# Optimization experiments

Hardware: AMD Instinct MI355X
Metric: run time of the kernel (lower is better)

## Reference

```python
import jax, jax.numpy as jnp
import numpy as np

# Multi-scale feature pyramid spatial shapes (h, w) per level; static for jit.
SPATIAL_SHAPES = np.array([[64, 176], [32, 88], [16, 44], [8, 22]], dtype=np.int32)


def setup_inputs() -> dict:
    key = jax.random.key(0)
    k1, k2 = jax.random.split(key)
    bs, num_heads, head_dim = 6, 8, 32          # 6 cams, embed_dim 256
    num_queries, num_levels, num_points = 40000, 4, 4  # 200x200 BEV grid, 4 Z anchors
    num_keys = int((SPATIAL_SHAPES[:, 0] * SPATIAL_SHAPES[:, 1]).sum())  # 14960
    value = jax.random.normal(k1, (bs, num_keys, num_heads, head_dim), jnp.float32)
    # normalized sampling locations in [0,1] (x, y)
    sampling_locations = jax.random.uniform(
        k2, (bs, num_queries, num_heads, num_levels, num_points, 2), jnp.float32)
    value_spatial_shapes = jnp.asarray(SPATIAL_SHAPES)
    return {"value": value,
            "value_spatial_shapes": value_spatial_shapes,
            "sampling_locations": sampling_locations}


def _msda(value, sampling_locations):
    """Multi-scale deformable attention, nearest sampling, zero padding,
    align_corners=False (matches F.grid_sample defaults used in the source).
    value: (bs, num_keys, H, D); sampling_locations: (bs, nq, H, L, P, 2).
    Returns (bs, nq, H*D)."""
    bs, _, H, D = value.shape
    _, nq, _, num_levels, P, _ = sampling_locations.shape
    grids = 2.0 * sampling_locations - 1.0  # -> [-1, 1]
    out = jnp.zeros((bs, H, nq, D), value.dtype)
    offset = 0
    for lvl in range(num_levels):
        h, w = int(SPATIAL_SHAPES[lvl, 0]), int(SPATIAL_SHAPES[lvl, 1])
        # (bs, h*w, H, D) -> (bs, H, h*w, D)
        v = jnp.transpose(value[:, offset:offset + h * w], (0, 2, 1, 3))
        g = grids[:, :, :, lvl]                      # (bs, nq, H, P, 2)
        # unnormalize (align_corners=False): pix = ((g+1)*size - 1)/2
        x = (g[..., 0] + 1.0) * w * 0.5 - 0.5
        y = (g[..., 1] + 1.0) * h * 0.5 - 0.5
        ix = jnp.rint(x).astype(jnp.int32)
        iy = jnp.rint(y).astype(jnp.int32)
        valid = (ix >= 0) & (ix < w) & (iy >= 0) & (iy < h)
        idx = jnp.clip(iy, 0, h - 1) * w + jnp.clip(ix, 0, w - 1)  # (bs, nq, H, P)
        idx = jnp.transpose(idx, (0, 2, 1, 3)).reshape(bs, H, nq * P)
        sampled = jnp.take_along_axis(v, idx[..., None], axis=2)  # (bs, H, nq*P, D)
        mask = jnp.transpose(valid, (0, 2, 1, 3)).reshape(bs, H, nq * P, 1)
        sampled = jnp.where(mask, sampled, 0.0).reshape(bs, H, nq, P, D)
        out = out + sampled.sum(axis=3)  # sum over points; accumulating over levels
        offset += h * w
    # (bs, H, nq, D) -> (bs, nq, H*D)
    return jnp.transpose(out, (0, 2, 1, 3)).reshape(bs, nq, H * D)


def reference(value, value_spatial_shapes, sampling_locations):
    # value_spatial_shapes matches the static SPATIAL_SHAPES constant used for
    # level splitting (shapes must be static under jit).
    return _msda(value, sampling_locations)
```

## Files before the change

### kernel.cpp

```cpp
#include <hip/hip_runtime.h>


#define BS 6
#define NQ 40000
#define NH 8
#define HD 32
#define NK 14960

__global__ __launch_bounds__(256)
void msda_kernel(const float* __restrict__ value,
                 const float* __restrict__ loc,
                 float* __restrict__ out) {
    constexpr int Wl[4]  = {176, 88, 44, 22};
    constexpr int Hl[4]  = {64, 32, 16, 8};
    constexpr int Off[4] = {0, 11264, 14080, 14784};

    const int tid = blockIdx.x * 256 + threadIdx.x;
    const int dg  = tid & 7;
    const int g   = tid >> 3;
    const int h   = g & 7;
    const int bq  = g >> 3;
    const int b   = bq / NQ;

    const float4* lp = (const float4*)(loc + (size_t)g * 32);
    const float* vbase = value + (size_t)b * (NK * NH * HD) + h * HD + dg * 4;

    float4 acc = make_float4(0.f, 0.f, 0.f, 0.f);

    #pragma unroll
    for (int l = 0; l < 4; ++l) {
        const int   W  = Wl[l], Hh = Hl[l], off = Off[l];
        const float wf = (float)W, hf = (float)Hh;
        #pragma unroll
        for (int i = 0; i < 2; ++i) {
            const float4 xy2 = lp[l * 2 + i];
            #pragma unroll
            for (int j = 0; j < 2; ++j) {
                const float px = j ? xy2.z : xy2.x;
                const float py = j ? xy2.w : xy2.y;
                const float gx = 2.0f * px - 1.0f;
                const float gy = 2.0f * py - 1.0f;
                const float x  = ((gx + 1.0f) * wf) * 0.5f - 0.5f;
                const float y  = ((gy + 1.0f) * hf) * 0.5f - 0.5f;
                const float fx = rintf(x);
                const float fy = rintf(y);
                const int ix = (int)fx;
                const int iy = (int)fy;
                const bool valid = (ix >= 0) & (ix < W) & (iy >= 0) & (iy < Hh);
                const int cx = min(max(ix, 0), W - 1);
                const int cy = min(max(iy, 0), Hh - 1);
                const int key = off + cy * W + cx;
                const float4 v = *(const float4*)(vbase + (size_t)key * (NH * HD));
                if (valid) {
                    acc.x += v.x; acc.y += v.y; acc.z += v.z; acc.w += v.w;
                }
            }
        }
    }

    *(float4*)(out + (size_t)g * HD + dg * 4) = acc;
}

extern "C" void kernel_launch(void* const* d_in, const int* in_sizes, int n_in,
                              void* d_out, int out_size, void* d_ws, size_t ws_size,
                              hipStream_t stream) {
    const float* value = (const float*)d_in[0];
    const float* loc   = (const float*)d_in[2];
    float* out = (float*)d_out;

    msda_kernel<<<60000, 256, 0, stream>>>(value, loc, out);
}
```

Before: 705.3 us.

## Split index math across lanes, broadcast offsets via shuffle, batch all gathers

Each of the 8 lanes sharing a (query, head) now computes sample indices for only one level/point pair instead of all 16, and the packed byte offsets plus valid bits are exchanged with wavefront shuffles. All 16 value gathers are then issued together, with an empty asm barrier that keeps them in flight at once. Masking becomes an FMA with a 0/1 weight. The aim is to remove redundant index computation and raise memory-level parallelism, at the cost of more registers (occupancy hint 4) and 32-bit unsigned addressing that assumes the value buffer fits in 4 GB.

```diff
diff --git a/kernel.cpp b/kernel.cpp
--- a/kernel.cpp
+++ b/kernel.cpp
@@ -7,14 +7,12 @@
 #define HD 32
 #define NK 14960
 
-__global__ __launch_bounds__(256)
+typedef float f32x4 __attribute__((ext_vector_type(4)));
+
+__global__ __launch_bounds__(256, 4)
 void msda_kernel(const float* __restrict__ value,
                  const float* __restrict__ loc,
                  float* __restrict__ out) {
-    constexpr int Wl[4]  = {176, 88, 44, 22};
-    constexpr int Hl[4]  = {64, 32, 16, 8};
-    constexpr int Off[4] = {0, 11264, 14080, 14784};
-
     const int tid = blockIdx.x * 256 + threadIdx.x;
     const int dg  = tid & 7;
     const int g   = tid >> 3;
@@ -22,43 +20,70 @@
     const int bq  = g >> 3;
     const int b   = bq / NQ;
 
-    const float4* lp = (const float4*)(loc + (size_t)g * 32);
-    const float* vbase = value + (size_t)b * (NK * NH * HD) + h * HD + dg * 4;
+    const int lane = threadIdx.x & 63;
+    const int ll   = lane & 7;
 
-    float4 acc = make_float4(0.f, 0.f, 0.f, 0.f);
+    const f32x4 myL = *(const f32x4*)(loc + (size_t)g * 32 + ll * 4);
 
+    const int l   = ll >> 1;
+    const int W   = 176 >> l;
+    const int Hh  = 64  >> l;
+    const int off = (45056 - (45056 >> (2 * l))) / 3;
+    const float wf = (float)W, hf = (float)Hh;
+
+    int koff[2];
     #pragma unroll
-    for (int l = 0; l < 4; ++l) {
-        const int   W  = Wl[l], Hh = Hl[l], off = Off[l];
-        const float wf = (float)W, hf = (float)Hh;
-        #pragma unroll
-        for (int i = 0; i < 2; ++i) {
-            const float4 xy2 = lp[l * 2 + i];
-            #pragma unroll
-            for (int j = 0; j < 2; ++j) {
-                const float px = j ? xy2.z : xy2.x;
-                const float py = j ? xy2.w : xy2.y;
-                const float gx = 2.0f * px - 1.0f;
-                const float gy = 2.0f * py - 1.0f;
-                const float x  = ((gx + 1.0f) * wf) * 0.5f - 0.5f;
-                const float y  = ((gy + 1.0f) * hf) * 0.5f - 0.5f;
-                const float fx = rintf(x);
-                const float fy = rintf(y);
-                const int ix = (int)fx;
-                const int iy = (int)fy;
-                const bool valid = (ix >= 0) & (ix < W) & (iy >= 0) & (iy < Hh);
-                const int cx = min(max(ix, 0), W - 1);
-                const int cy = min(max(iy, 0), Hh - 1);
-                const int key = off + cy * W + cx;
-                const float4 v = *(const float4*)(vbase + (size_t)key * (NH * HD));
-                if (valid) {
-                    acc.x += v.x; acc.y += v.y; acc.z += v.z; acc.w += v.w;
-                }
-            }
-        }
+    for (int j = 0; j < 2; ++j) {
+        const float px = j ? myL.z : myL.x;
+        const float py = j ? myL.w : myL.y;
+        const float gx = 2.0f * px - 1.0f;
+        const float gy = 2.0f * py - 1.0f;
+        const float x  = ((gx + 1.0f) * wf) * 0.5f - 0.5f;
+        const float y  = ((gy + 1.0f) * hf) * 0.5f - 0.5f;
+        const float fx = rintf(x);
+        const float fy = rintf(y);
+        const int ix = (int)fx;
+        const int iy = (int)fy;
+        const bool valid = (ix >= 0) & (ix < W) & (iy >= 0) & (iy < Hh);
+        const int cx = min(max(ix, 0), W - 1);
+        const int cy = min(max(iy, 0), Hh - 1);
+        const int key = off + cy * W + cx;
+        koff[j] = (key << 10) | (valid ? 1 : 0);
     }
 
-    *(float4*)(out + (size_t)g * HD + dg * 4) = acc;
+    const int srcbase = lane & 56;
+    int ko[16];
+    #pragma unroll
+    for (int s = 0; s < 16; ++s)
+        ko[s] = __shfl(koff[s & 1], srcbase + (s >> 1), 64);
+
+    const unsigned base_off = (unsigned)b * (NK * NH * HD * 4u)
+                            + (unsigned)h * (HD * 4u)
+                            + (unsigned)dg * 16u;
+
+    f32x4 v[16];
+    #pragma unroll
+    for (int s = 0; s < 16; ++s) {
+        const unsigned a = base_off + ((unsigned)ko[s] & 0xFFFFFFFEu);
+        v[s] = *(const f32x4*)((const char*)value + a);
+    }
+    asm volatile(""
+        : "+v"(v[0]),  "+v"(v[1]),  "+v"(v[2]),  "+v"(v[3]),
+          "+v"(v[4]),  "+v"(v[5]),  "+v"(v[6]),  "+v"(v[7]),
+          "+v"(v[8]),  "+v"(v[9]),  "+v"(v[10]), "+v"(v[11]),
+          "+v"(v[12]), "+v"(v[13]), "+v"(v[14]), "+v"(v[15]));
+
+    f32x4 acc = {0.f, 0.f, 0.f, 0.f};
+    #pragma unroll
+    for (int s = 0; s < 16; ++s) {
+        const float w = (float)(ko[s] & 1);
+        acc.x = fmaf(v[s].x, w, acc.x);
+        acc.y = fmaf(v[s].y, w, acc.y);
+        acc.z = fmaf(v[s].z, w, acc.z);
+        acc.w = fmaf(v[s].w, w, acc.w);
+    }
+
+    *(f32x4*)(out + (size_t)g * HD + dg * 4) = acc;
 }
 
 extern "C" void kernel_launch(void* const* d_in, const int* in_sizes, int n_in,
```

Result: faster. 620.6 us (-12.0%).

## Persistent per-head blocks with LDS-staged small levels and software-pipelined gathers

Applied to the files above, without the earlier changes.

Each block now handles one (batch, head) pair over 1600 queries. Blocks map to XCDs by head so each XCD's L2 holds one head's value slice, and the two small pyramid levels for that head are staged once into LDS. The 8 lanes of a query each compute one pair of sample indices and share them with __shfl. Global gathers for the next query are issued ahead, locations are prefetched two iterations ahead with nontemporal loads, and masking becomes an FMA with a 0/1 weight. This targets redundant index math, scattered global traffic and L2 locality, at the cost of higher register pressure and a hard-coded grid decomposition.

```diff
diff --git a/kernel.cpp b/kernel.cpp
--- a/kernel.cpp
+++ b/kernel.cpp
@@ -7,58 +7,160 @@
 #define HD 32
 #define NK 14960
 
-__global__ __launch_bounds__(256)
+#define STAGE_KEY0 14080
+#define STAGE_KEYS 880
+#define THREADS    512
+#define QPT        25
+#define QPB        1600
+
+typedef float f32x4 __attribute__((ext_vector_type(4)));
+
+__global__ __launch_bounds__(THREADS, 2)
 void msda_kernel(const float* __restrict__ value,
                  const float* __restrict__ loc,
                  float* __restrict__ out) {
-    constexpr int Wl[4]  = {176, 88, 44, 22};
-    constexpr int Hl[4]  = {64, 32, 16, 8};
-    constexpr int Off[4] = {0, 11264, 14080, 14784};
+    extern __shared__ float lds[];
 
-    const int tid = blockIdx.x * 256 + threadIdx.x;
-    const int dg  = tid & 7;
-    const int g   = tid >> 3;
-    const int h   = g & 7;
-    const int bq  = g >> 3;
-    const int b   = bq / NQ;
+    const int t    = threadIdx.x;
+    const int ll   = t & 7;
+    const int gr   = t >> 3;
+    const int lane = t & 63;
 
-    const float4* lp = (const float4*)(loc + (size_t)g * 32);
-    const float* vbase = value + (size_t)b * (NK * NH * HD) + h * HD + dg * 4;
+    const int xcd   = blockIdx.x & 7;
+    const int seq   = blockIdx.x >> 3;
+    const int b     = seq / 25;
+    const int chunk = seq - b * 25;
+    const int h     = xcd;
+    const int qbase = chunk * QPB;
 
-    float4 acc = make_float4(0.f, 0.f, 0.f, 0.f);
+    const char* vb = (const char*)value;
+    const size_t vbh = (size_t)b * (NK * 1024) + (size_t)h * 128;
 
-    #pragma unroll
-    for (int l = 0; l < 4; ++l) {
-        const int   W  = Wl[l], Hh = Hl[l], off = Off[l];
-        const float wf = (float)W, hf = (float)Hh;
+    {
+        const char* src0 = vb + vbh + (size_t)STAGE_KEY0 * 1024;
         #pragma unroll
-        for (int i = 0; i < 2; ++i) {
-            const float4 xy2 = lp[l * 2 + i];
-            #pragma unroll
-            for (int j = 0; j < 2; ++j) {
-                const float px = j ? xy2.z : xy2.x;
-                const float py = j ? xy2.w : xy2.y;
-                const float gx = 2.0f * px - 1.0f;
-                const float gy = 2.0f * py - 1.0f;
-                const float x  = ((gx + 1.0f) * wf) * 0.5f - 0.5f;
-                const float y  = ((gy + 1.0f) * hf) * 0.5f - 0.5f;
-                const float fx = rintf(x);
-                const float fy = rintf(y);
-                const int ix = (int)fx;
-                const int iy = (int)fy;
-                const bool valid = (ix >= 0) & (ix < W) & (iy >= 0) & (iy < Hh);
-                const int cx = min(max(ix, 0), W - 1);
-                const int cy = min(max(iy, 0), Hh - 1);
-                const int key = off + cy * W + cx;
-                const float4 v = *(const float4*)(vbase + (size_t)key * (NH * HD));
-                if (valid) {
-                    acc.x += v.x; acc.y += v.y; acc.z += v.z; acc.w += v.w;
-                }
+        for (int k = 0; k < 14; ++k) {
+            const int i = t + k * THREADS;
+            if (i < STAGE_KEYS * 8) {
+                const int key8 = i >> 3, part = i & 7;
+                const f32x4 d = *(const f32x4*)(src0 + (size_t)key8 * 1024 + part * 16);
+                *(f32x4*)(lds + (size_t)i * 4) = d;
             }
         }
     }
+    __syncthreads();
 
-    *(float4*)(out + (size_t)g * HD + dg * 4) = acc;
+    const int   l     = ll >> 1;
+    const int   W     = 176 >> l;
+    const int   Hh    = 64  >> l;
+    const float wf    = (float)W, hf = (float)Hh;
+    const bool  isglb = (l < 2);
+    const int   lvlbase = isglb ? (l == 0 ? 0 : 11264) : (l == 2 ? 0 : 704);
+    const int   shmul   = isglb ? 1024 : 128;
+
+    auto compute2 = [&](const f32x4 Lv, int* kp) {
+        #pragma unroll
+        for (int j = 0; j < 2; ++j) {
+            const float px = j ? Lv.z : Lv.x;
+            const float py = j ? Lv.w : Lv.y;
+            const float gx = 2.0f * px - 1.0f;
+            const float gy = 2.0f * py - 1.0f;
+            const float x  = ((gx + 1.0f) * wf) * 0.5f - 0.5f;
+            const float y  = ((gy + 1.0f) * hf) * 0.5f - 0.5f;
+            const float fx = rintf(x);
+            const float fy = rintf(y);
+            const int ix = (int)fx;
+            const int iy = (int)fy;
+            const bool valid = (ix >= 0) & (ix < W) & (iy >= 0) & (iy < Hh);
+            const int cx = min(max(ix, 0), W - 1);
+            const int cy = min(max(iy, 0), Hh - 1);
+            kp[j] = (lvlbase + cy * W + cx) * shmul + (valid ? 1 : 0);
+        }
+    };
+
+    auto locAddr = [&](int qi) {
+        const int q = qbase + qi * 64 + gr;
+        return (const f32x4*)(loc + ((size_t)(b * NQ + q) * NH + h) * 32 + ll * 4);
+    };
+
+    const int srcbase = lane & 56;
+    const char* vlane = vb + vbh + ll * 16;
+    const char* lbase = (const char*)lds + ll * 16;
+
+    f32x4 Lnext = __builtin_nontemporal_load(locAddr(0));
+    f32x4 Lfar  = __builtin_nontemporal_load(locAddr(1));
+    int   koG[8], koL[8];
+    float wG[8], wL[8];
+    {
+        int kp[2];
+        compute2(Lnext, kp);
+        #pragma unroll
+        for (int s = 0; s < 16; ++s) {
+            const int a = __shfl(kp[s & 1], srcbase + (s >> 1), 64);
+            if (s < 8) { koG[s]     = a & ~1; wG[s]     = (float)(a & 1); }
+            else       { koL[s - 8] = a & ~1; wL[s - 8] = (float)(a & 1); }
+        }
+    }
+    Lnext = Lfar;
+    f32x4 vg[8];
+    #pragma unroll
+    for (int s = 0; s < 8; ++s)
+        vg[s] = *(const f32x4*)(vlane + (unsigned)koG[s]);
+
+    #pragma unroll 1
+    for (int qi = 0; qi < QPT; ++qi) {
+        f32x4 vl[8];
+        #pragma unroll
+        for (int s = 0; s < 8; ++s)
+            vl[s] = *(const f32x4*)(lbase + (unsigned)koL[s]);
+
+        int   koG2[8], koL2[8];
+        float wG2[8], wL2[8];
+        if (qi + 1 < QPT) {
+            int kp[2];
+            compute2(Lnext, kp);
+            #pragma unroll
+            for (int s = 0; s < 16; ++s) {
+                const int a = __shfl(kp[s & 1], srcbase + (s >> 1), 64);
+                if (s < 8) { koG2[s]     = a & ~1; wG2[s]     = (float)(a & 1); }
+                else       { koL2[s - 8] = a & ~1; wL2[s - 8] = (float)(a & 1); }
+            }
+        }
+
+        if (qi + 2 < QPT) Lfar = __builtin_nontemporal_load(locAddr(qi + 2));
+
+        f32x4 acc = {0.f, 0.f, 0.f, 0.f};
+        #pragma unroll
+        for (int s = 0; s < 8; ++s) {
+            acc.x = fmaf(vg[s].x, wG[s], acc.x);
+            acc.y = fmaf(vg[s].y, wG[s], acc.y);
+            acc.z = fmaf(vg[s].z, wG[s], acc.z);
+            acc.w = fmaf(vg[s].w, wG[s], acc.w);
+        }
+        #pragma unroll
+        for (int s = 0; s < 8; ++s) {
+            acc.x = fmaf(vl[s].x, wL[s], acc.x);
+            acc.y = fmaf(vl[s].y, wL[s], acc.y);
+            acc.z = fmaf(vl[s].z, wL[s], acc.z);
+            acc.w = fmaf(vl[s].w, wL[s], acc.w);
+        }
+
+        const int q = qbase + qi * 64 + gr;
+        __builtin_nontemporal_store(acc,
+            (f32x4*)(out + ((size_t)(b * NQ + q) * NH + h) * 32 + ll * 4));
+
+        if (qi + 1 < QPT) {
+            #pragma unroll
+            for (int s = 0; s < 8; ++s) {
+                koG[s] = koG2[s]; wG[s] = wG2[s];
+                koL[s] = koL2[s]; wL[s] = wL2[s];
+            }
+            #pragma unroll
+            for (int s = 0; s < 8; ++s)
+                vg[s] = *(const f32x4*)(vlane + (unsigned)koG[s]);
+            Lnext = Lfar;
+        }
+    }
 }
 
 extern "C" void kernel_launch(void* const* d_in, const int* in_sizes, int n_in,
@@ -68,5 +170,5 @@
     const float* loc   = (const float*)d_in[2];
     float* out = (float*)d_out;
 
-    msda_kernel<<<60000, 256, 0, stream>>>(value, loc, out);
+    msda_kernel<<<1200, THREADS, STAGE_KEYS * 128, stream>>>(value, loc, out);
 }
```

Result: faster. 608.2 us (-13.8%).
